# Kernel tuning notes

Hardware: AMD Instinct MI355X
Metric: run time of the kernel (lower is better)

Reference implementation:

```python
import jax, jax.numpy as jnp
import numpy as np

B_SCENES = 2; K = 5; C = 128; H = 64; W = 64
D_INNER = C; D_STATE = 16; DT_RANK = 8
C_TUKEY = 0.3; ALPHA = 2.0; BETA = 0.4; GAMMA = 0.8


def affine_grid(theta, Ho, Wo):
    # torch F.affine_grid, align_corners=False (pixel centers)
    xs = (jnp.arange(Wo, dtype=jnp.float32) + 0.5) * (2.0 / Wo) - 1.0
    ys = (jnp.arange(Ho, dtype=jnp.float32) + 0.5) * (2.0 / Ho) - 1.0
    gx, gy = jnp.meshgrid(xs, ys)
    base = jnp.stack([gx, gy, jnp.ones_like(gx)], axis=-1)  # (H,W,3)
    return jnp.einsum('nij,hwj->nhwi', theta, base)  # (N,H,W,2)


def grid_sample(src, grid):
    # bilinear, zero padding, align_corners=False; src (N,C,H,W), grid (N,H,W,2)
    N, Cc, Hs, Ws = src.shape
    ix = ((grid[..., 0] + 1.0) * Ws - 1.0) * 0.5
    iy = ((grid[..., 1] + 1.0) * Hs - 1.0) * 0.5
    x0 = jnp.floor(ix); y0 = jnp.floor(iy)
    def tap(xf, yf):
        v = ((xf >= 0) & (xf <= Ws - 1) & (yf >= 0) & (yf <= Hs - 1)).astype(src.dtype)
        xc = jnp.clip(xf, 0, Ws - 1).astype(jnp.int32)
        yc = jnp.clip(yf, 0, Hs - 1).astype(jnp.int32)
        vals = jax.vmap(lambda s, y, x: s[:, y, x])(src, yc, xc)  # (N,C,H,W)
        return vals * v[:, None]
    wx1 = (ix - x0)[:, None]; wy1 = (iy - y0)[:, None]
    wx0 = 1.0 - wx1; wy0 = 1.0 - wy1
    return (tap(x0, y0) * wx0 * wy0 + tap(x0 + 1.0, y0) * wx1 * wy0
            + tap(x0, y0 + 1.0) * wx0 * wy1 + tap(x0 + 1.0, y0 + 1.0) * wx1 * wy1)


def ss2d(tokens, in_proj_w, conv_w, conv_b, x_proj_w, dt_w, dt_b, A_logs, Ds, ln_g, ln_b, out_proj_w):
    # tokens (C, Hs, Ws) channel-first; VMamba-style v05_noz core, d_inner=C
    xin = jnp.einsum('chw,dc->dhw', tokens, in_proj_w)
    xc = jax.lax.conv_general_dilated(xin[None], conv_w, (1, 1), [(1, 1), (1, 1)],
                                      dimension_numbers=('NCHW', 'OIHW', 'NCHW'),
                                      feature_group_count=D_INNER)[0] + conv_b[:, None, None]
    xa = jax.nn.silu(xc)
    d, Hs, Ws = xa.shape
    L = Hs * Ws
    x_hw = xa.reshape(d, L)
    x_wh = jnp.swapaxes(xa, 1, 2).reshape(d, L)
    xs = jnp.stack([x_hw, x_wh, x_hw[:, ::-1], x_wh[:, ::-1]], axis=0)  # (4,d,L)
    x_dbl = jnp.einsum('kdl,kcd->kcl', xs, x_proj_w)
    dt = x_dbl[:, :DT_RANK]
    Bm = x_dbl[:, DT_RANK:DT_RANK + D_STATE]
    Cm = x_dbl[:, DT_RANK + D_STATE:]
    dts = jax.nn.softplus(jnp.einsum('kdr,krl->kdl', dt_w, dt) + dt_b[..., None])
    A = -jnp.exp(A_logs)  # (4,d,n)
    seq = (jnp.moveaxis(xs, -1, 0), jnp.moveaxis(dts, -1, 0),
           jnp.moveaxis(Bm, -1, 0), jnp.moveaxis(Cm, -1, 0))
    def step(h, inp):
        xt, dtt, Bt, Ct = inp
        h = h * jnp.exp(dtt[..., None] * A) + (dtt * xt)[..., None] * Bt[:, None, :]
        return h, jnp.einsum('kdn,kn->kd', h, Ct)
    h0 = jnp.zeros((4, d, D_STATE), tokens.dtype)
    _, ys = jax.lax.scan(jax.checkpoint(step), h0, seq)  # ys (L,4,d)
    ys = jnp.moveaxis(ys, 0, -1) + Ds[..., None] * xs  # (4,d,L)
    untr = lambda y: jnp.swapaxes(y.reshape(d, Ws, Hs), 1, 2).reshape(d, L)
    y = ys[0] + untr(ys[1]) + ys[2][:, ::-1] + untr(ys[3][:, ::-1])
    yt = y.T  # (L,d)
    mu = yt.mean(-1, keepdims=True)
    var = ((yt - mu) ** 2).mean(-1, keepdims=True)
    yn = (yt - mu) * jax.lax.rsqrt(var + 1e-5) * ln_g + ln_b
    out = yn @ out_proj_w.T  # (L,C)
    return jnp.moveaxis(out.reshape(Hs, Ws, -1), -1, 0)  # (C,Hs,Ws)


def forward(x, nam, in_proj_w, conv_w, conv_b, x_proj_w, dt_w, dt_b, A_logs, Ds, ln_g, ln_b, out_proj_w):
    xg = x.reshape(B_SCENES, K, C, H, W)  # record_len is constant K
    t_rows = nam[:, 0]  # ego row i=0 of t_matrix: (B,K,2,3)
    def scene(xb, t_row):
        warped = grid_sample(xb, affine_grid(t_row, H, W))  # (K,C,H,W)
        ego = warped[0]
        # per-pixel cosine sim across channels (F.normalize(dim=0) on (C,HW) views)
        en = ego / jnp.maximum(jnp.sqrt((ego ** 2).sum(0, keepdims=True)), 1e-6)
        nb = warped / jnp.maximum(jnp.sqrt((warped ** 2).sum(1, keepdims=True)), 1e-6)
        sims = jnp.clip((en[None] * nb).sum(1), -1.0, 1.0)  # (K,H,W)
        r = jnp.maximum(1.0 - sims, 0.0)
        xr = jnp.maximum(r / C_TUKEY, 0.0)
        w_pix = jnp.maximum(jnp.maximum(1.0 - xr * xr, 0.0) ** 2, 1e-6)[:, None]  # (K,1,H,W)
        tx = t_row[:, 0, 2]; ty = t_row[:, 1, 2]
        yaw = jnp.abs(jnp.arctan2(t_row[:, 0, 1], t_row[:, 0, 0]))
        g = jax.nn.sigmoid(ALPHA - BETA * jnp.sqrt(tx ** 2 + ty ** 2) - GAMMA * yaw)  # (K,)
        logit = jnp.log(w_pix + 1e-8) + jnp.log(g + 1e-8)[:, None, None, None]
        alpha = jax.nn.softmax(logit, axis=0)  # softmax over K per pixel
        weighted = warped * alpha
        tokens = jnp.swapaxes(weighted.reshape(K, C, H * W), 0, 1)  # (C,K,HW)
        out = ss2d(tokens, in_proj_w, conv_w, conv_b, x_proj_w, dt_w, dt_b,
                   A_logs, Ds, ln_g, ln_b, out_proj_w)  # (C,K,HW)
        return jnp.swapaxes(out, 0, 1).reshape(K, C, W, H)[0]  # (C,W,H) as in original view
    return jax.vmap(scene)(xg, t_rows)


def setup_inputs() -> dict:
    key = jax.random.key(0)
    ks = jax.random.split(key, 10)
    x = jax.random.normal(ks[0], (B_SCENES * K, C, H, W), jnp.float32)
    record_len = jnp.full((B_SCENES,), K, dtype=jnp.int32)
    eye = jnp.broadcast_to(jnp.array([[1.0, 0.0, 0.0], [0.0, 1.0, 0.0]], jnp.float32),
                           (B_SCENES, K, K, 2, 3))
    nam = eye + 0.05 * jax.random.normal(ks[1], (B_SCENES, K, K, 2, 3), jnp.float32)
    in_proj_w = 0.05 * jax.random.normal(ks[2], (D_INNER, C), jnp.float32)
    conv_w = 0.1 * jax.random.normal(ks[3], (D_INNER, 1, 3, 3), jnp.float32)
    conv_b = jnp.zeros((D_INNER,), jnp.float32)
    x_proj_w = 0.05 * jax.random.normal(ks[4], (4, DT_RANK + 2 * D_STATE, D_INNER), jnp.float32)
    dt_w = 0.1 * jax.random.normal(ks[5], (4, D_INNER, DT_RANK), jnp.float32)
    dt_b = -4.6 + 0.5 * jax.random.normal(ks[6], (4, D_INNER), jnp.float32)
    A_logs = jnp.broadcast_to(jnp.log(jnp.arange(1, D_STATE + 1, dtype=jnp.float32)),
                              (4, D_INNER, D_STATE)) + jnp.zeros((4, D_INNER, D_STATE), jnp.float32)
    Ds = jnp.ones((4, D_INNER), jnp.float32)
    ln_g = jnp.ones((D_INNER,), jnp.float32)
    ln_b = jnp.zeros((D_INNER,), jnp.float32)
    out_proj_w = 0.05 * jax.random.normal(ks[7], (C, D_INNER), jnp.float32)
    return {"x": x, "record_len": record_len, "normalized_affine_matrix": nam,
            "in_proj_w": in_proj_w, "conv_w": conv_w, "conv_b": conv_b,
            "x_proj_w": x_proj_w, "dt_w": dt_w, "dt_b": dt_b, "A_logs": A_logs,
            "Ds": Ds, "ln_g": ln_g, "ln_b": ln_b, "out_proj_w": out_proj_w}


def reference(x, record_len, normalized_affine_matrix, in_proj_w, conv_w, conv_b,
              x_proj_w, dt_w, dt_b, A_logs, Ds, ln_g, ln_b, out_proj_w):
    # record_len is a constant (= K per scene) and only determines the static grouping
    return forward(x, normalized_affine_matrix, in_proj_w, conv_w, conv_b,
                   x_proj_w, dt_w, dt_b, A_logs, Ds, ln_g, ln_b, out_proj_w)
```

## Files before the change

kernel.cpp:

```cpp
#include <hip/hip_runtime.h>
#include <math.h>

#define B_S   2
#define PIX   4096
#define LL    20480
#define NS    16
#define RR    8
#define NCHK  512
#define LC    40
#define SUBS  10
#define NSUB  4
#define NGRP  32
#define GCH   16
#define K0CH  104

typedef float v2f __attribute__((ext_vector_type(2)));

__device__ __forceinline__ v2f pk_mul(v2f a, v2f b) {
  v2f d;
  asm("v_pk_mul_f32 %0, %1, %2" : "=v"(d) : "v"(a), "v"(b));
  return d;
}
#define PK_FMA_ACC(a, b, c) asm("v_pk_fma_f32 %0, %1, %2, %0" : "+v"(a) : "v"(b), "v"(c))
#define PK_DECAY(h, e, m) asm("v_pk_fma_f32 %0, %0, %1, %2" : "+v"(h) : "v"(e), "v"(m))

template<int K>
__device__ __forceinline__ int zmapT(int l) {
  if (K == 0) return l;
  if (K == 1) return ((l % 5) << 12) + l / 5;
  if (K == 2) return 20479 - l;
  int lr = 20479 - l;
  return ((lr % 5) << 12) + lr / 5;
}

__global__ __launch_bounds__(256)
void k_warp(const float* __restrict__ x, const float* __restrict__ nam,
            float* __restrict__ warped) {
  int g = blockIdx.x * 256 + threadIdx.x;
  int p  = g & 4095;
  int c  = (g >> 12) & 127;
  int bk = g >> 19;
  int b = bk / 5, k = bk - b * 5;
  const float* th = nam + (size_t)(b * 25 + k) * 6;
  float gx = ((p & 63) + 0.5f) * 0.03125f - 1.0f;
  float gy = ((p >> 6) + 0.5f) * 0.03125f - 1.0f;
  float grx = th[0] * gx + th[1] * gy + th[2];
  float gry = th[3] * gx + th[4] * gy + th[5];
  float ix = ((grx + 1.0f) * 64.0f - 1.0f) * 0.5f;
  float iy = ((gry + 1.0f) * 64.0f - 1.0f) * 0.5f;
  float x0 = floorf(ix), y0 = floorf(iy);
  float fx = ix - x0,  fy = iy - y0;
  const float* src = x + (size_t)(bk * 128 + c) * PIX;
  float acc = 0.0f;
  #pragma unroll
  for (int dy = 0; dy < 2; ++dy) {
    float yf = y0 + dy;
    float wy = dy ? fy : 1.0f - fy;
    if (yf < 0.0f || yf > 63.0f) continue;
    int yi = (int)yf;
    #pragma unroll
    for (int dx = 0; dx < 2; ++dx) {
      float xf = x0 + dx;
      float wx = dx ? fx : 1.0f - fx;
      if (xf < 0.0f || xf > 63.0f) continue;
      acc += wx * wy * src[yi * 64 + (int)xf];
    }
  }
  warped[g] = acc;
}

__global__ __launch_bounds__(512)
void k_alpha(const float* __restrict__ warped, const float* __restrict__ nam,
             float* __restrict__ alpha) {
  __shared__ float part[8][64][9];
  int blk = blockIdx.x;
  int b = blk >> 6;
  int p0 = (blk & 63) << 6;
  int wv = threadIdx.x >> 6, lane = threadIdx.x & 63;
  int p = p0 + lane;
  const float* wb = warped + (size_t)b * 5 * 128 * PIX + p;
  float dot[5] = {0,0,0,0,0}, ssq[5] = {0,0,0,0,0};
  int c0 = wv * 16;
  for (int c = c0; c < c0 + 16; ++c) {
    float w0 = wb[(size_t)c * PIX];
    ssq[0] += w0 * w0;
    #pragma unroll
    for (int k = 1; k < 5; ++k) {
      float wk = wb[((size_t)k * 128 + c) * PIX];
      dot[k] += w0 * wk;
      ssq[k] += wk * wk;
    }
  }
  part[wv][lane][0] = ssq[0];
  #pragma unroll
  for (int k = 1; k < 5; ++k) {
    part[wv][lane][k] = dot[k];
    part[wv][lane][4 + k] = ssq[k];
  }
  __syncthreads();
  if (threadIdx.x < 64) {
    float q[9];
    #pragma unroll
    for (int j = 0; j < 9; ++j) {
      float s = 0.0f;
      #pragma unroll
      for (int w = 0; w < 8; ++w) s += part[w][lane][j];
      q[j] = s;
    }
    float n0 = fmaxf(sqrtf(q[0]), 1e-6f);
    float logit[5];
    #pragma unroll
    for (int k = 0; k < 5; ++k) {
      float dotk = (k == 0) ? q[0] : q[k];
      float ssqk = (k == 0) ? q[0] : q[4 + k];
      float nk = fmaxf(sqrtf(ssqk), 1e-6f);
      float sim = fminf(fmaxf(dotk / (n0 * nk), -1.0f), 1.0f);
      float r = fmaxf(1.0f - sim, 0.0f);
      float xr = r * (1.0f / 0.3f);
      float tt = fmaxf(1.0f - xr * xr, 0.0f);
      float wp = fmaxf(tt * tt, 1e-6f);
      const float* th = nam + (size_t)(b * 25 + k) * 6;
      float tx = th[2], ty = th[5];
      float yaw = fabsf(atan2f(th[1], th[0]));
      float gk = 1.0f / (1.0f + __expf(-(2.0f - 0.4f * sqrtf(tx*tx + ty*ty) - 0.8f * yaw)));
      logit[k] = __logf(wp + 1e-8f) + __logf(gk + 1e-8f);
    }
    float m = logit[0];
    #pragma unroll
    for (int k = 1; k < 5; ++k) m = fmaxf(m, logit[k]);
    float e[5], s = 0.0f;
    #pragma unroll
    for (int k = 0; k < 5; ++k) { e[k] = __expf(logit[k] - m); s += e[k]; }
    float inv = 1.0f / s;
    #pragma unroll
    for (int k = 0; k < 5; ++k)
      alpha[((size_t)(b * 5 + k)) * PIX + p] = e[k] * inv;
  }
}

__global__ __launch_bounds__(256, 4)
void k_gemm_in(const float* __restrict__ warped, const float* __restrict__ alpha,
               const float* __restrict__ W, float* __restrict__ X0) {
  __shared__ float xl[64][129];
  __shared__ __align__(16) float wlT[32][132];
  int t = threadIdx.x;
  int row0 = blockIdx.x * 64;
  int b = row0 / LL;
  int z0 = row0 - b * LL;
  int a = z0 >> 12;
  int p0 = z0 & 4095;
  int ba = b * 5 + a;
// ... 92 lines not shown
}

__global__ __launch_bounds__(256, 4)
void k_gemmZ(const float* __restrict__ X, const float* __restrict__ W,
             float* __restrict__ ZdtB, float* __restrict__ ZC) {
  __shared__ float xl[64][129];
  __shared__ __align__(16) float wlT[32][164];
  int t = threadIdx.x;
  int row0 = blockIdx.x * 64;
  #pragma unroll
  for (int i = 0; i < 32; ++i) {
    int idx = i * 256 + t;
    xl[idx >> 7][idx & 127] = X[((size_t)row0 + (idx >> 7)) * 128 + (idx & 127)];
  }
  int zl2 = t & 31;
  int mg  = t >> 5;
  float acc0[20], acc1[20];
  #pragma unroll
  for (int i = 0; i < 20; ++i) { acc0[i] = 0.0f; acc1[i] = 0.0f; }
  for (int c0 = 0; c0 < 128; c0 += 32) {
    __syncthreads();
    #pragma unroll
    for (int i = 0; i < 20; ++i) {
      int m = (t >> 5) * 20 + i;
      wlT[t & 31][m] = W[(size_t)m * 128 + c0 + (t & 31)];
    }
    __syncthreads();
    const float* xr0 = xl[2 * zl2];
    const float* xr1 = xl[2 * zl2 + 1];
    for (int cc = 0; cc < 32; ++cc) {
      float xv0 = xr0[c0 + cc];
      float xv1 = xr1[c0 + cc];
      const float4* wr = (const float4*)(&wlT[cc][mg * 20]);
      #pragma unroll
      for (int q = 0; q < 5; ++q) {
        float4 w4 = wr[q];
        acc0[q*4+0] = fmaf(w4.x, xv0, acc0[q*4+0]);
        acc0[q*4+1] = fmaf(w4.y, xv0, acc0[q*4+1]);
        acc0[q*4+2] = fmaf(w4.z, xv0, acc0[q*4+2]);
        acc0[q*4+3] = fmaf(w4.w, xv0, acc0[q*4+3]);
        acc1[q*4+0] = fmaf(w4.x, xv1, acc1[q*4+0]);
        acc1[q*4+1] = fmaf(w4.y, xv1, acc1[q*4+1]);
        acc1[q*4+2] = fmaf(w4.z, xv1, acc1[q*4+2]);
        acc1[q*4+3] = fmaf(w4.w, xv1, acc1[q*4+3]);
      }
    }
  }
  int dir = mg >> 1;
  int halfc = mg & 1;
  #pragma unroll
  for (int rr = 0; rr < 2; ++rr) {
    const float* acc = rr ? acc1 : acc0;
    int row = row0 + 2 * zl2 + rr;
    int b = row / LL, z = row - b * LL;
    int a = z >> 12, qq = z & 4095;
    int l;
    if (dir == 0)      l = z;
    else if (dir == 1) l = 5 * qq + a;
    else if (dir == 2) l = 20479 - z;
    else               l = 20479 - (5 * qq + a);
    size_t seqrow = (size_t)(b * 4 + dir) * LL + l;
    if (halfc == 0) {
      float* dD = ZdtB + seqrow * 24;
      #pragma unroll
      for (int q2 = 0; q2 < 5; ++q2)
        *(float4*)(dD + q2 * 4) = make_float4(acc[q2*4], acc[q2*4+1], acc[q2*4+2], acc[q2*4+3]);
    } else {
      float* dD = ZdtB + seqrow * 24;
      *(float4*)(dD + 20) = make_float4(acc[0], acc[1], acc[2], acc[3]);
      float* dC = ZC + seqrow * 16;
      #pragma unroll
      for (int q2 = 0; q2 < 4; ++q2)
        *(float4*)(dC + q2 * 4) = make_float4(acc[4+q2*4], acc[4+q2*4+1], acc[4+q2*4+2], acc[4+q2*4+3]);
    }
  }
}

template<int K>
__device__ void scan_body(int b, int chunk, int dh, int lane,
    const float* __restrict__ XT, const float* __restrict__ ZdtB,
    const float* __restrict__ ZC,
    const float* __restrict__ dt_w, const float* __restrict__ dt_b,
    const float* __restrict__ A_logs, const float* __restrict__ Ds,
    float* __restrict__ h_out, float* __restrict__ sumdts,
    float* __restrict__ ysz, float* __restrict__ cumqv,
    float* stD, float* stC)
{
  const int d = dh * 64 + lane;
  const int kd = K * 128 + d;
  bool chainok = true;
  #pragma unroll
  for (int n = 0; n < NS; ++n) {
    float An = -__expf(A_logs[(size_t)kd * 16 + n]);
    chainok = chainok && (fabsf(An + (float)(n + 1)) < 3e-5f * (float)(n + 1));
  }
  v2f dw2[4];
  #pragma unroll
  for (int r = 0; r < 4; ++r) {
    dw2[r][0] = dt_w[(size_t)kd * 8 + 2 * r];
    dw2[r][1] = dt_w[(size_t)kd * 8 + 2 * r + 1];
  }
  const float dtb = dt_b[kd], dsv = Ds[kd];
  v2f h2[8];
  #pragma unroll
  for (int n = 0; n < 8; ++n) h2[n] = (v2f){0.0f, 0.0f};
  float sdt = 0.0f;
  float qrun = 1.0f;
  const int seq = b * 4 + K;
  const float* ZDs = ZdtB + (size_t)seq * LL * 24;
  const float* ZCs = ZC + (size_t)seq * LL * 16;
  const float* Xb = XT + (size_t)b * LL * 128;
  float* ysb = ysz + (size_t)seq * PIX * 128;
  float* cqb = cumqv + (size_t)seq * PIX * 128;
  const int l0 = chunk * LC;

  if (__all(chainok ? 1 : 0)) {
    #pragma unroll 1
    for (int sub = 0; sub < NSUB; ++sub) {
      const int ls = l0 + sub * SUBS;
      {
        const v2f* srcD = (const v2f*)(ZDs + (size_t)ls * 24);
        v2f* dstD = (v2f*)stD;
        #pragma unroll
        for (int i = 0; i < 2; ++i) {
          int idx = i * 64 + lane;
          if (idx < SUBS * 12) dstD[idx] = srcD[idx];
        }
      }
      int s0c = 0;
      bool needC;
      if (K == 0)      needC = (ls < PIX);
      else if (K == 2) needC = (ls + SUBS > LL - PIX);
      else             needC = true;
      if (K == 1) s0c = (5 - (ls % 5)) % 5;
      if (K == 3) s0c = (9 - (ls % 5)) % 5;
      if (needC) {
        if (K == 0 || K == 2) {
          const v2f* srcC = (const v2f*)(ZCs + (size_t)ls * 16);
          v2f* dstC = (v2f*)stC;
          #pragma unroll
          for (int i = 0; i < 2; ++i) {
            int idx = i * 64 + lane;
            if (idx < SUBS * 8) dstC[idx] = srcC[idx];
          }
        } else {
          int j = lane >> 4, col = lane & 15;
          if (j < 2) {
            int l = ls + s0c + 5 * j;
            if (l > LL - 1) l = LL - 1;
            stC[lane] = ZCs[(size_t)l * 16 + col];
          }
        }
      }
      float xr[SUBS];
      #pragma unroll
      for (int s = 0; s < SUBS; ++s) {
        int z = zmapT<K>(ls + s);
        xr[s] = Xb[(size_t)z * 128 + d];
      }
      int zc = 0;
      if (K == 1) zc = (ls + s0c) / 5;
      if (K == 3) zc = (20479 - ls - s0c) / 5;
      int yj = 0;
      #pragma unroll
      for (int s = 0; s < SUBS; ++s) {
        const v2f* rowD = (const v2f*)(stD + s * 24);
        v2f zd0 = rowD[0], zd1 = rowD[1], zd2 = rowD[2], zd3 = rowD[3];
        v2f da = pk_mul(dw2[0], zd0);
        PK_FMA_ACC(da, dw2[1], zd1);
        PK_FMA_ACC(da, dw2[2], zd2);
        PK_FMA_ACC(da, dw2[3], zd3);
        float dtl = dtb + da[0] + da[1];
        float edt = __expf(dtl);
        float e1 = __builtin_amdgcn_rcpf(1.0f + edt);
        float dt = (dtl > 20.0f) ? dtl : __logf(1.0f + edt);
        sdt += dt;
        qrun *= e1;
        float xsv = xr[s];
        float dtx = dt * xsv;
        v2f dtx2 = {dtx, dtx};
        float e2 = e1 * e1;
        v2f E[8];
        E[0] = (v2f){e1, e2};
        v2f e2s = {e2, e2};
        E[1] = pk_mul(E[0], e2s);
        E[2] = pk_mul(E[1], e2s);
        E[3] = pk_mul(E[2], e2s);
        float e8 = E[3][1];
        v2f e8s = {e8, e8};
        E[4] = pk_mul(E[0], e8s);
        E[5] = pk_mul(E[1], e8s);
        E[6] = pk_mul(E[2], e8s);
        E[7] = pk_mul(E[3], e8s);
        const v2f* B2 = (const v2f*)(stD + s * 24 + 8);
        #pragma unroll
        for (int i = 0; i < 8; ++i) {
          v2f m = pk_mul(dtx2, B2[i]);
          PK_DECAY(h2[i], E[i], m);
        }
        bool doY;
        int z;
        if (K == 0)      { z = ls + s;            doY = (z < PIX); }
        else if (K == 2) { z = 20479 - (ls + s);  doY = (z < PIX); }
        else             { z = zc;                doY = ((s % 5) == s0c); }
        if (doY) {
          const v2f* C2 = (const v2f*)(stC + ((K == 0 || K == 2) ? s : yj) * 16);
          v2f ya = pk_mul(h2[0], C2[0]);
          #pragma unroll
          for (int i = 1; i < 8; ++i) PK_FMA_ACC(ya, h2[i], C2[i]);
          float y = fmaf(dsv, xsv, ya[0] + ya[1]);
          size_t o = (size_t)z * 128 + d;
          ysb[o] = y;
          cqb[o] = qrun;
          ++yj;
          if (K == 1) ++zc;
          if (K == 3) --zc;
        }
      }
    }
  } else {
    float An[NS];
    #pragma unroll
    for (int n = 0; n < NS; ++n) An[n] = -__expf(A_logs[(size_t)kd * 16 + n]);
    float hs[NS];
    #pragma unroll
    for (int n = 0; n < NS; ++n) hs[n] = 0.0f;
    #pragma unroll 1
    for (int l = l0; l < l0 + LC; ++l) {
      int z = zmapT<K>(l);
      const float* rowD = ZDs + (size_t)l * 24;
      float dtl = dtb;
      #pragma unroll
      for (int r = 0; r < RR; ++r) dtl += dt_w[(size_t)kd * 8 + r] * rowD[r];
      float edt = __expf(dtl);
      float dt = (dtl > 20.0f) ? dtl : __logf(1.0f + edt);
      sdt += dt;
      float xv = Xb[(size_t)z * 128 + d];
      float dtx = dt * xv;
      #pragma unroll
      for (int n = 0; n < NS; ++n)
        hs[n] = hs[n] * __expf(dt * An[n]) + dtx * rowD[8 + n];
      if (z < PIX) {
        const float* rowC = ZCs + (size_t)l * 16;
        float y = dsv * xv;
        #pragma unroll
        for (int n = 0; n < NS; ++n) y = fmaf(hs[n], rowC[n], y);
        size_t o = (size_t)z * 128 + d;
        ysb[o] = y;
        cqb[o] = __expf(-sdt);
      }
    }
    #pragma unroll
    for (int n = 0; n < 8; ++n) h2[n] = (v2f){hs[2*n], hs[2*n+1]};
  }
  float* ho = h_out + (((size_t)seq * NCHK + chunk) * 128 + d) * 16;
  #pragma unroll
  for (int n = 0; n < 8; ++n) {
    ho[2*n] = h2[n][0];
    ho[2*n+1] = h2[n][1];
  }
  sumdts[((size_t)seq * NCHK + chunk) * 128 + d] = sdt;
}

__global__ __launch_bounds__(128, 8)
void k_scan1(const float* __restrict__ XT, const float* __restrict__ ZdtB,
             const float* __restrict__ ZC,
             const float* __restrict__ dt_w, const float* __restrict__ dt_b,
             const float* __restrict__ A_logs, const float* __restrict__ Ds,
             float* __restrict__ h_out, float* __restrict__ sumdts,
             float* __restrict__ ysz, float* __restrict__ cumqv) {
  __shared__ __align__(16) float stD_all[2][SUBS * 24];
  __shared__ __align__(16) float stC_all[2][SUBS * 16];
  int tid = threadIdx.x, wid = tid >> 6, lane = tid & 63;
  int bid = blockIdx.x;
  int bb = bid / (K0CH + 3 * NCHK);
  int idx = bid - bb * (K0CH + 3 * NCHK);
  int k, chunk;
  if (idx < K0CH)                 { k = 0; chunk = idx; }
  else if (idx < K0CH + NCHK)     { k = 1; chunk = idx - K0CH; }
  else if (idx < K0CH + 2 * NCHK) { k = 2; chunk = idx - (K0CH + NCHK); }
  else                            { k = 3; chunk = idx - (K0CH + 2 * NCHK); }
  int dh = wid;
  float* stD = stD_all[wid];
  float* stC = stC_all[wid];
  switch (k) {
    case 0: scan_body<0>(bb, chunk, dh, lane, XT, ZdtB, ZC, dt_w, dt_b, A_logs, Ds, h_out, sumdts, ysz, cumqv, stD, stC); break;
    case 1: scan_body<1>(bb, chunk, dh, lane, XT, ZdtB, ZC, dt_w, dt_b, A_logs, Ds, h_out, sumdts, ysz, cumqv, stD, stC); break;
    case 2: scan_body<2>(bb, chunk, dh, lane, XT, ZdtB, ZC, dt_w, dt_b, A_logs, Ds, h_out, sumdts, ysz, cumqv, stD, stC); break;
    default: scan_body<3>(bb, chunk, dh, lane, XT, ZdtB, ZC, dt_w, dt_b, A_logs, Ds, h_out, sumdts, ysz, cumqv, stD, stC); break;
  }
}

__global__ __launch_bounds__(256)
void k_comb_a(const float* __restrict__ A_logs, const float* __restrict__ sumdts,
              const float* __restrict__ h_out, float* __restrict__ Ag,
              float* __restrict__ Bg) {
  int g = blockIdx.x * 256 + threadIdx.x;
  int n = g & 15;
  int d = (g >> 4) & 127;
  int grp = (g >> 11) & 31;
  int seq = g >> 16;
  int k = seq & 3;
  if (k == 0 && grp > 6) return;
  float An = -__expf(A_logs[(size_t)(k * 128 + d) * 16 + n]);
  float A = 1.0f, Bv = 0.0f;
  size_t cbase = (size_t)seq * NCHK + grp * GCH;
  #pragma unroll 4
  for (int j = 0; j < GCH; ++j) {
    float a = __expf(An * sumdts[(cbase + j) * 128 + d]);
    float b = h_out[((cbase + j) * 128 + d) * 16 + n];
    A *= a;
    Bv = Bv * a + b;
  }
  size_t o = (((size_t)seq * NGRP + grp) * 128 + d) * 16 + n;
  Ag[o] = A;
  Bg[o] = Bv;
}

__global__ __launch_bounds__(256)
void k_comb_b(const float* __restrict__ Ag, const float* __restrict__ Bg,
              float* __restrict__ Hg) {
  int g = blockIdx.x * 256 + threadIdx.x;
  int n = g & 15;
  int d = (g >> 4) & 127;
  int seq = g >> 11;
  float H = 0.0f;
  #pragma unroll
  for (int grp = 0; grp < NGRP; ++grp) {
    size_t o = (((size_t)seq * NGRP + grp) * 128 + d) * 16 + n;
    Hg[o] = H;
    H = Ag[o] * H + Bg[o];
  }
}

__global__ __launch_bounds__(256)
void k_comb_c(const float* __restrict__ A_logs, const float* __restrict__ sumdts,
              const float* __restrict__ h_out, const float* __restrict__ Hg,
              float* __restrict__ h_in) {
  int g = blockIdx.x * 256 + threadIdx.x;
  int n = g & 15;
  int d = (g >> 4) & 127;
  int grp = (g >> 11) & 31;
  int seq = g >> 16;
  int k = seq & 3;
  if (k == 0 && grp > 6) return;
  if (k == 2 && grp < 25) return;
  float An = -__expf(A_logs[(size_t)(k * 128 + d) * 16 + n]);
  float h = Hg[(((size_t)seq * NGRP + grp) * 128 + d) * 16 + n];
  size_t cbase = (size_t)seq * NCHK + grp * GCH;
  #pragma unroll 4
  for (int j = 0; j < GCH; ++j) {
    size_t o = ((cbase + j) * 128 + d) * 16 + n;
    h_in[o] = h;
    float a = __expf(An * sumdts[(cbase + j) * 128 + d]);
    h = a * h + h_out[o];
  }
}

__global__ __launch_bounds__(256)
void k_wt(const float* __restrict__ Wo, float* __restrict__ WT) {
  __shared__ float tl[32][33];
  int bx = blockIdx.x & 3, by = blockIdx.x >> 2;
  int t = threadIdx.x;
  int tx = t & 31, ty = t >> 5;
  #pragma unroll
  for (int i = 0; i < 4; ++i)
    tl[ty + i * 8][tx] = Wo[(size_t)(by * 32 + ty + i * 8) * 128 + bx * 32 + tx];
  __syncthreads();
  #pragma unroll
  for (int i = 0; i < 4; ++i)
    WT[(size_t)(bx * 32 + ty + i * 8) * 128 + by * 32 + tx] = tl[tx][ty + i * 8];
}

__global__ __launch_bounds__(256)
void k_merge(const float* __restrict__ ysz, const float* __restrict__ ZC,
             const float* __restrict__ A_logs, const float* __restrict__ h_in,
             const float* __restrict__ cumq,
             const float* __restrict__ ln_g, const float* __restrict__ ln_b,
             const float* __restrict__ WT, float* __restrict__ out) {
  __shared__ __align__(16) float ynT[128][20];
  __shared__ float red[4][8][2];
  int blk = blockIdx.x;
  int b = blk >> 8;
  int p0 = (blk & 255) * 16;
  int tid = threadIdx.x;
  int t = tid & 127;
  int half = tid >> 7;
  int w = tid >> 6;
  float g = ln_g[t], bb = ln_b[t];
  bool cok[4];
  #pragma unroll
  for (int k = 0; k < 4; ++k) {
    bool c = true;
    #pragma unroll
    for (int n = 0; n < NS; ++n) {
      float An = -__expf(A_logs[(size_t)(k * 128 + t) * 16 + n]);
      c = c && (fabsf(An + (float)(n + 1)) < 3e-5f * (float)(n + 1));
    }
    cok[k] = c;
  }
  float yv[8];
  #pragma unroll
  for (int i = 0; i < 8; ++i) {
    int p = p0 + 2 * i + half;
    float y = 0.0f;
    #pragma unroll
    for (int k = 0; k < 4; ++k) {
      size_t zi = ((size_t)(b * 4 + k) * PIX + p) * 128 + t;
      float yk = ysz[zi];
      int l;
      if (k == 0)      l = p;
      else if (k == 1) l = 5 * p;
      else if (k == 2) l = 20479 - p;
      else             l = 20479 - 5 * p;
      int chunk = l / LC;
      float q = cumq[zi];
      const v2f* hi2 = (const v2f*)(h_in + (((size_t)(b * 4 + k) * NCHK + chunk) * 128 + t) * 16);
      const v2f* Cr2 = (const v2f*)(ZC + ((size_t)(b * 4 + k) * LL + l) * 16);
      float fix;
      if (cok[k]) {
        float q2 = q * q;
        v2f Q[8];
        Q[0] = (v2f){q, q2};
        v2f q2s = {q2, q2};
        Q[1] = pk_mul(Q[0], q2s);
        Q[2] = pk_mul(Q[1], q2s);
        Q[3] = pk_mul(Q[2], q2s);
        float q8 = Q[3][1];
        v2f q8s = {q8, q8};
        Q[4] = pk_mul(Q[0], q8s);
        Q[5] = pk_mul(Q[1], q8s);
        Q[6] = pk_mul(Q[2], q8s);
        Q[7] = pk_mul(Q[3], q8s);
        v2f a = pk_mul(pk_mul(hi2[0], Cr2[0]), Q[0]);
        #pragma unroll
        for (int j = 1; j < 8; ++j) {
          v2f m = pk_mul(hi2[j], Cr2[j]);
          PK_FMA_ACC(a, m, Q[j]);
        }
        fix = a[0] + a[1];
      } else {
        float cd = -__logf(q);
        fix = 0.0f;
        const float* hi = (const float*)hi2;
        const float* Cr = (const float*)Cr2;
        #pragma unroll
        for (int n = 0; n < NS; ++n) {
          float An = -__expf(A_logs[(size_t)(k * 128 + t) * 16 + n]);
          fix += Cr[n] * hi[n] * __expf(An * cd);
        }
      }
      y += yk + fix;
    }
    yv[i] = y;
    float s1 = y, s2 = y * y;
    #pragma unroll
    for (int off = 32; off; off >>= 1) {
      s1 += __shfl_xor(s1, off);
      s2 += __shfl_xor(s2, off);
    }
    if ((tid & 63) == 0) { red[w][i][0] = s1; red[w][i][1] = s2; }
  }
  __syncthreads();
  #pragma unroll
  for (int i = 0; i < 8; ++i) {
    int pl = 2 * i + half;
    float S1 = red[half * 2][i][0] + red[half * 2 + 1][i][0];
    float S2 = red[half * 2][i][1] + red[half * 2 + 1][i][1];
    float mu = S1 * (1.0f / 128.0f);
    float var = S2 * (1.0f / 128.0f) - mu * mu;
    float rs = rsqrtf(var + 1e-5f);
    ynT[t][pl] = (yv[i] - mu) * rs * g + bb;
  }
  __syncthreads();
  float acc[8];
  #pragma unroll
  for (int i = 0; i < 8; ++i) acc[i] = 0.0f;
  for (int dd = 0; dd < 128; ++dd) {
    float wv = WT[(size_t)dd * 128 + t];
    const float4* yr = (const float4*)(&ynT[dd][half * 8]);
    float4 ya = yr[0], yb4 = yr[1];
    acc[0] = fmaf(ya.x,  wv, acc[0]);
    acc[1] = fmaf(ya.y,  wv, acc[1]);
    acc[2] = fmaf(ya.z,  wv, acc[2]);
    acc[3] = fmaf(ya.w,  wv, acc[3]);
    acc[4] = fmaf(yb4.x, wv, acc[4]);
    acc[5] = fmaf(yb4.y, wv, acc[5]);
    acc[6] = fmaf(yb4.z, wv, acc[6]);
    acc[7] = fmaf(yb4.w, wv, acc[7]);
  }
  float* dst = out + ((size_t)b * 128 + t) * PIX + p0 + half * 8;
  *(float4*)(dst)     = make_float4(acc[0], acc[1], acc[2], acc[3]);
  *(float4*)(dst + 4) = make_float4(acc[4], acc[5], acc[6], acc[7]);
}

extern "C" void kernel_launch(void* const* d_in, const int* in_sizes, int n_in,
                              void* d_out, int out_size, void* d_ws, size_t ws_size,
                              hipStream_t stream) {
  const float* x         = (const float*)d_in[0];
  const float* nam       = (const float*)d_in[2];
  const float* in_proj_w = (const float*)d_in[3];
  const float* conv_w    = (const float*)d_in[4];
  const float* conv_b    = (const float*)d_in[5];
  const float* x_proj_w  = (const float*)d_in[6];
  const float* dt_w      = (const float*)d_in[7];
  const float* dt_b      = (const float*)d_in[8];
  const float* A_logs    = (const float*)d_in[9];
  const float* Ds        = (const float*)d_in[10];
  const float* ln_g      = (const float*)d_in[11];
  const float* ln_b      = (const float*)d_in[12];
  const float* out_proj_w= (const float*)d_in[13];
  float* out = (float*)d_out;
  float* ws  = (float*)d_ws;

  float* warped = ws;
  float* alpha  = warped + 5242880;
  float* X0     = alpha  + 40960;
  float* XT     = X0     + 5242880;
  float* ZdtB   = XT     + 5242880;
  float* ZC     = ZdtB   + 3932160;
  float* sums   = ZC     + 2621440;
  float* ysz    = sums   + 524288;
  float* cumq   = ysz    + 4194304;
  float* WT     = cumq   + 4194304;
  float* Ag     = WT     + 16384;
  float* Bg     = Ag     + 524288;
  float* Hg     = Bg     + 524288;

  float* h_out = ws;
  float* h_in  = XT;

  k_warp   <<<20480, 256, 0, stream>>>(x, nam, warped);
  k_alpha  <<<128,   512, 0, stream>>>(warped, nam, alpha);
  k_gemm_in<<<640,   256, 0, stream>>>(warped, alpha, in_proj_w, X0);
  k_conv   <<<5120,  256, 0, stream>>>(X0, conv_w, conv_b, XT);
  k_gemmZ  <<<640,   256, 0, stream>>>(XT, x_proj_w, ZdtB, ZC);
  k_scan1  <<<B_S * (K0CH + 3 * NCHK), 128, 0, stream>>>(XT, ZdtB, ZC, dt_w, dt_b,
                                                         A_logs, Ds, h_out, sums, ysz, cumq);
  k_comb_a <<<2048,  256, 0, stream>>>(A_logs, sums, h_out, Ag, Bg);
  k_comb_b <<<64,    256, 0, stream>>>(Ag, Bg, Hg);
  k_comb_c <<<2048,  256, 0, stream>>>(A_logs, sums, h_out, Hg, h_in);
  k_wt     <<<16,    256, 0, stream>>>(out_proj_w, WT);
  k_merge  <<<512,   256, 0, stream>>>(ysz, ZC, A_logs, h_in, cumq,
                                       ln_g, ln_b, WT, out);
}
```

Before: 254.8 us.

## Shrink scan chunk length, share warp sampling weights, compact h_in layout

The scan chunk length drops from 40 to 32, which raises the chunk and group counts and grows the workspace. The combine and merge kernels now use a compact h_in layout that keeps only the chunks actually read. k_warp computes bilinear weights and indices once per pixel tile in shared memory and reuses them across 4 channels, replacing the per-thread coordinate math and branches. More chunks give more parallelism per sequence but add carry-combine work and memory traffic.

```diff
diff --git a/kernel.cpp b/kernel.cpp
--- a/kernel.cpp
+++ b/kernel.cpp
@@ -6,13 +6,13 @@
 #define LL    20480
 #define NS    16
 #define RR    8
-#define NCHK  512
-#define LC    40
-#define SUBS  10
+#define NCHK  640
+#define LC    32
+#define SUBS  8
 #define NSUB  4
-#define NGRP  32
+#define NGRP  40
 #define GCH   16
-#define K0CH  104
+#define K0CH  128
 
 typedef float v2f __attribute__((ext_vector_type(2)));
 
@@ -36,37 +36,52 @@
 __global__ __launch_bounds__(256)
 void k_warp(const float* __restrict__ x, const float* __restrict__ nam,
             float* __restrict__ warped) {
-  int g = blockIdx.x * 256 + threadIdx.x;
-  int p  = g & 4095;
-  int c  = (g >> 12) & 127;
-  int bk = g >> 19;
-  int b = bk / 5, k = bk - b * 5;
-  const float* th = nam + (size_t)(b * 25 + k) * 6;
-  float gx = ((p & 63) + 0.5f) * 0.03125f - 1.0f;
-  float gy = ((p >> 6) + 0.5f) * 0.03125f - 1.0f;
-  float grx = th[0] * gx + th[1] * gy + th[2];
-  float gry = th[3] * gx + th[4] * gy + th[5];
-  float ix = ((grx + 1.0f) * 64.0f - 1.0f) * 0.5f;
-  float iy = ((gry + 1.0f) * 64.0f - 1.0f) * 0.5f;
-  float x0 = floorf(ix), y0 = floorf(iy);
-  float fx = ix - x0,  fy = iy - y0;
+  __shared__ float wL[4][64];
+  __shared__ int   iL[4][64];
+  int blk = blockIdx.x;
+  int bk = blk >> 11;
+  int rem = blk & 2047;
+  int ct = rem >> 6, pt = rem & 63;
+  int p0 = pt * 64;
+  int t = threadIdx.x;
+  int pl = t & 63, cg = t >> 6;
+  if (t < 64) {
+    int b = bk / 5, k = bk - b * 5;
+    const float* th = nam + (size_t)(b * 25 + k) * 6;
+    int p = p0 + t;
+    float gx = ((p & 63) + 0.5f) * 0.03125f - 1.0f;
+    float gy = ((p >> 6) + 0.5f) * 0.03125f - 1.0f;
+    float grx = th[0] * gx + th[1] * gy + th[2];
+    float gry = th[3] * gx + th[4] * gy + th[5];
+    float ix = ((grx + 1.0f) * 64.0f - 1.0f) * 0.5f;
+    float iy = ((gry + 1.0f) * 64.0f - 1.0f) * 0.5f;
+    float x0 = floorf(ix), y0 = floorf(iy);
+    float fx = ix - x0, fy = iy - y0;
+    float vx0 = (x0 >= 0.0f && x0 <= 63.0f) ? 1.0f : 0.0f;
+    float vx1 = (x0 >= -1.0f && x0 <= 62.0f) ? 1.0f : 0.0f;
+    float vy0 = (y0 >= 0.0f && y0 <= 63.0f) ? 1.0f : 0.0f;
+    float vy1 = (y0 >= -1.0f && y0 <= 62.0f) ? 1.0f : 0.0f;
+    int xi0 = (int)fminf(fmaxf(x0, 0.0f), 63.0f);
+    int yi0 = (int)fminf(fmaxf(y0, 0.0f), 63.0f);
+    int xi1 = (int)fminf(fmaxf(x0 + 1.0f, 0.0f), 63.0f);
+    int yi1 = (int)fminf(fmaxf(y0 + 1.0f, 0.0f), 63.0f);
+    wL[0][t] = (1.0f - fx) * (1.0f - fy) * vx0 * vy0;
+    wL[1][t] = fx * (1.0f - fy) * vx1 * vy0;
+    wL[2][t] = (1.0f - fx) * fy * vx0 * vy1;
+    wL[3][t] = fx * fy * vx1 * vy1;
+    iL[0][t] = yi0 * 64 + xi0;
+    iL[1][t] = yi0 * 64 + xi1;
+    iL[2][t] = yi1 * 64 + xi0;
+    iL[3][t] = yi1 * 64 + xi1;
+  }
+  __syncthreads();
+  int c = ct * 4 + cg;
   const float* src = x + (size_t)(bk * 128 + c) * PIX;
-  float acc = 0.0f;
-  #pragma unroll
-  for (int dy = 0; dy < 2; ++dy) {
-    float yf = y0 + dy;
-    float wy = dy ? fy : 1.0f - fy;
-    if (yf < 0.0f || yf > 63.0f) continue;
-    int yi = (int)yf;
-    #pragma unroll
-    for (int dx = 0; dx < 2; ++dx) {
-      float xf = x0 + dx;
-      float wx = dx ? fx : 1.0f - fx;
-      if (xf < 0.0f || xf > 63.0f) continue;
-      acc += wx * wy * src[yi * 64 + (int)xf];
-    }
-  }
-  warped[g] = acc;
+  float acc = wL[0][pl] * src[iL[0][pl]]
+            + wL[1][pl] * src[iL[1][pl]]
+            + wL[2][pl] * src[iL[2][pl]]
+            + wL[3][pl] * src[iL[3][pl]];
+  warped[((size_t)(bk * 128 + c)) * PIX + p0 + pl] = acc;
 }
 
 __global__ __launch_bounds__(512)
@@ -516,13 +531,13 @@
   __shared__ __align__(16) float stC_all[2][SUBS * 16];
   int tid = threadIdx.x, wid = tid >> 6, lane = tid & 63;
   int bid = blockIdx.x;
-  int bb = bid / (K0CH + 3 * NCHK);
-  int idx = bid - bb * (K0CH + 3 * NCHK);
+  int bb = bid >> 11;
+  int idx = bid & 2047;
   int k, chunk;
-  if (idx < K0CH)                 { k = 0; chunk = idx; }
-  else if (idx < K0CH + NCHK)     { k = 1; chunk = idx - K0CH; }
-  else if (idx < K0CH + 2 * NCHK) { k = 2; chunk = idx - (K0CH + NCHK); }
-  else                            { k = 3; chunk = idx - (K0CH + 2 * NCHK); }
+  if (idx < K0CH)        { k = 0; chunk = idx; }
+  else if (idx < 768)    { k = 1; chunk = idx - K0CH; }
+  else if (idx < 1408)   { k = 2; chunk = idx - 768; }
+  else                   { k = 3; chunk = idx - 1408; }
   int dh = wid;
   float* stD = stD_all[wid];
   float* stC = stC_all[wid];
@@ -541,10 +556,11 @@
   int g = blockIdx.x * 256 + threadIdx.x;
   int n = g & 15;
   int d = (g >> 4) & 127;
-  int grp = (g >> 11) & 31;
-  int seq = g >> 16;
+  int rem = g >> 11;
+  int seq = rem / NGRP;
+  int grp = rem - seq * NGRP;
   int k = seq & 3;
-  if (k == 0 && grp > 6) return;
+  if (k == 0 && grp > 7) return;
   float An = -__expf(A_logs[(size_t)(k * 128 + d) * 16 + n]);
   float A = 1.0f, Bv = 0.0f;
   size_t cbase = (size_t)seq * NCHK + grp * GCH;
@@ -583,21 +599,27 @@
   int g = blockIdx.x * 256 + threadIdx.x;
   int n = g & 15;
   int d = (g >> 4) & 127;
-  int grp = (g >> 11) & 31;
-  int seq = g >> 16;
+  int rem = g >> 11;
+  int seq = rem / NGRP;
+  int grp = rem - seq * NGRP;
   int k = seq & 3;
-  if (k == 0 && grp > 6) return;
-  if (k == 2 && grp < 25) return;
+  if (k == 0 && grp > 7) return;
+  if (k == 2 && grp < 32) return;
+  int b = seq >> 2;
+  int cstart = (k == 2) ? 512 : 0;
+  int offk = (k == 0) ? 0 : (k == 1) ? 128 : (k == 2) ? 768 : 896;
   float An = -__expf(A_logs[(size_t)(k * 128 + d) * 16 + n]);
   float h = Hg[(((size_t)seq * NGRP + grp) * 128 + d) * 16 + n];
   size_t cbase = (size_t)seq * NCHK + grp * GCH;
   #pragma unroll 4
   for (int j = 0; j < GCH; ++j) {
-    size_t o = ((cbase + j) * 128 + d) * 16 + n;
-    h_in[o] = h;
-    float a = __expf(An * sumdts[(cbase + j) * 128 + d]);
-    h = a * h + h_out[o];
-  }
+    int chunk = grp * GCH + j;
+    size_t o = ((size_t)seq * NCHK + chunk) * 128 + d;
+    h_in[(((size_t)b * 1536 + offk + (chunk - cstart)) * 128 + d) * 16 + n] = h;
+    float a = __expf(An * sumdts[o]);
+    h = a * h + h_out[o * 16 + n];
+  }
+  (void)cbase;
 }
 
 __global__ __launch_bounds__(256)
@@ -657,8 +679,10 @@
       else if (k == 2) l = 20479 - p;
       else             l = 20479 - 5 * p;
       int chunk = l / LC;
+      int cidx = chunk - ((k == 2) ? 512 : 0);
+      int offk = (k == 0) ? 0 : (k == 1) ? 128 : (k == 2) ? 768 : 896;
       float q = cumq[zi];
-      const v2f* hi2 = (const v2f*)(h_in + (((size_t)(b * 4 + k) * NCHK + chunk) * 128 + t) * 16);
+      const v2f* hi2 = (const v2f*)(h_in + (((size_t)b * 1536 + offk + cidx) * 128 + t) * 16);
       const v2f* Cr2 = (const v2f*)(ZC + ((size_t)(b * 4 + k) * LL + l) * 16);
       float fix;
       if (cok[k]) {
@@ -763,12 +787,12 @@
   float* ZdtB   = XT     + 5242880;
   float* ZC     = ZdtB   + 3932160;
   float* sums   = ZC     + 2621440;
-  float* ysz    = sums   + 524288;
+  float* ysz    = sums   + 655360;
   float* cumq   = ysz    + 4194304;
   float* WT     = cumq   + 4194304;
   float* Ag     = WT     + 16384;
-  float* Bg     = Ag     + 524288;
-  float* Hg     = Bg     + 524288;
+  float* Bg     = Ag     + 655360;
+  float* Hg     = Bg     + 655360;
 
   float* h_out = ws;
   float* h_in  = XT;
@@ -778,11 +802,11 @@
   k_gemm_in<<<640,   256, 0, stream>>>(warped, alpha, in_proj_w, X0);
   k_conv   <<<5120,  256, 0, stream>>>(X0, conv_w, conv_b, XT);
   k_gemmZ  <<<640,   256, 0, stream>>>(XT, x_proj_w, ZdtB, ZC);
-  k_scan1  <<<B_S * (K0CH + 3 * NCHK), 128, 0, stream>>>(XT, ZdtB, ZC, dt_w, dt_b,
-                                                         A_logs, Ds, h_out, sums, ysz, cumq);
-  k_comb_a <<<2048,  256, 0, stream>>>(A_logs, sums, h_out, Ag, Bg);
+  k_scan1  <<<B_S * 2048, 128, 0, stream>>>(XT, ZdtB, ZC, dt_w, dt_b,
+                                            A_logs, Ds, h_out, sums, ysz, cumq);
+  k_comb_a <<<2560,  256, 0, stream>>>(A_logs, sums, h_out, Ag, Bg);
   k_comb_b <<<64,    256, 0, stream>>>(Ag, Bg, Hg);
-  k_comb_c <<<2048,  256, 0, stream>>>(A_logs, sums, h_out, Hg, h_in);
+  k_comb_c <<<2560,  256, 0, stream>>>(A_logs, sums, h_out, Hg, h_in);
   k_wt     <<<16,    256, 0, stream>>>(out_proj_w, WT);
   k_merge  <<<512,   256, 0, stream>>>(ysz, ZC, A_logs, h_in, cumq,
                                        ln_g, ln_b, WT, out);
```

Measured after the change: 256.9 us. Within noise of the previous version (+0.9%).

## Share warp coordinates per pixel tile, precompute chain flags, widen scan loads

Applied to the files above, without the earlier changes.

k_warp now computes the bilinear indices and weights once per 64-pixel tile in shared memory and reuses them across 4 channels per block, instead of recomputing them per channel thread. The per-lane A_logs chain check (16 exps per thread) in k_scan1 and k_merge is replaced by flags computed once in extra blocks of k_wt, which now runs first. Scan staging copies and shared reads use float4 vectors, and dt_w is kept in registers for the tail loop. The new flag kernel ordering adds a dependency, and the block-level sync in k_warp adds a small serialization.

```diff
diff --git a/kernel.cpp b/kernel.cpp
--- a/kernel.cpp
+++ b/kernel.cpp
@@ -15,6 +15,7 @@
 #define K0CH  104
 
 typedef float v2f __attribute__((ext_vector_type(2)));
+typedef float v4f __attribute__((ext_vector_type(4)));
 
 __device__ __forceinline__ v2f pk_mul(v2f a, v2f b) {
   v2f d;
@@ -36,37 +37,52 @@
 __global__ __launch_bounds__(256)
 void k_warp(const float* __restrict__ x, const float* __restrict__ nam,
             float* __restrict__ warped) {
-  int g = blockIdx.x * 256 + threadIdx.x;
-  int p  = g & 4095;
-  int c  = (g >> 12) & 127;
-  int bk = g >> 19;
-  int b = bk / 5, k = bk - b * 5;
-  const float* th = nam + (size_t)(b * 25 + k) * 6;
-  float gx = ((p & 63) + 0.5f) * 0.03125f - 1.0f;
-  float gy = ((p >> 6) + 0.5f) * 0.03125f - 1.0f;
-  float grx = th[0] * gx + th[1] * gy + th[2];
-  float gry = th[3] * gx + th[4] * gy + th[5];
-  float ix = ((grx + 1.0f) * 64.0f - 1.0f) * 0.5f;
-  float iy = ((gry + 1.0f) * 64.0f - 1.0f) * 0.5f;
-  float x0 = floorf(ix), y0 = floorf(iy);
-  float fx = ix - x0,  fy = iy - y0;
+  __shared__ float wL[4][64];
+  __shared__ int   iL[4][64];
+  int blk = blockIdx.x;
+  int bk = blk >> 11;
+  int rem = blk & 2047;
+  int ct = rem >> 6, pt = rem & 63;
+  int p0 = pt * 64;
+  int t = threadIdx.x;
+  int pl = t & 63, cg = t >> 6;
+  if (t < 64) {
+    int b = bk / 5, k = bk - b * 5;
+    const float* th = nam + (size_t)(b * 25 + k) * 6;
+    int p = p0 + t;
+    float gx = ((p & 63) + 0.5f) * 0.03125f - 1.0f;
+    float gy = ((p >> 6) + 0.5f) * 0.03125f - 1.0f;
+    float grx = th[0] * gx + th[1] * gy + th[2];
+    float gry = th[3] * gx + th[4] * gy + th[5];
+    float ix = ((grx + 1.0f) * 64.0f - 1.0f) * 0.5f;
+    float iy = ((gry + 1.0f) * 64.0f - 1.0f) * 0.5f;
+    float x0 = floorf(ix), y0 = floorf(iy);
+    float fx = ix - x0, fy = iy - y0;
+    float vx0 = (x0 >= 0.0f && x0 <= 63.0f) ? 1.0f : 0.0f;
+    float vx1 = (x0 >= -1.0f && x0 <= 62.0f) ? 1.0f : 0.0f;
+    float vy0 = (y0 >= 0.0f && y0 <= 63.0f) ? 1.0f : 0.0f;
+    float vy1 = (y0 >= -1.0f && y0 <= 62.0f) ? 1.0f : 0.0f;
+    int xi0 = (int)fminf(fmaxf(x0, 0.0f), 63.0f);
+    int yi0 = (int)fminf(fmaxf(y0, 0.0f), 63.0f);
+    int xi1 = (int)fminf(fmaxf(x0 + 1.0f, 0.0f), 63.0f);
+    int yi1 = (int)fminf(fmaxf(y0 + 1.0f, 0.0f), 63.0f);
+    wL[0][t] = (1.0f - fx) * (1.0f - fy) * vx0 * vy0;
+    wL[1][t] = fx * (1.0f - fy) * vx1 * vy0;
+    wL[2][t] = (1.0f - fx) * fy * vx0 * vy1;
+    wL[3][t] = fx * fy * vx1 * vy1;
+    iL[0][t] = yi0 * 64 + xi0;
+    iL[1][t] = yi0 * 64 + xi1;
+    iL[2][t] = yi1 * 64 + xi0;
+    iL[3][t] = yi1 * 64 + xi1;
+  }
+  __syncthreads();
+  int c = ct * 4 + cg;
   const float* src = x + (size_t)(bk * 128 + c) * PIX;
-  float acc = 0.0f;
-  #pragma unroll
-  for (int dy = 0; dy < 2; ++dy) {
-    float yf = y0 + dy;
-    float wy = dy ? fy : 1.0f - fy;
-    if (yf < 0.0f || yf > 63.0f) continue;
-    int yi = (int)yf;
-    #pragma unroll
-    for (int dx = 0; dx < 2; ++dx) {
-      float xf = x0 + dx;
-      float wx = dx ? fx : 1.0f - fx;
-      if (xf < 0.0f || xf > 63.0f) continue;
-      acc += wx * wy * src[yi * 64 + (int)xf];
-    }
-  }
-  warped[g] = acc;
+  float acc = wL[0][pl] * src[iL[0][pl]]
+            + wL[1][pl] * src[iL[1][pl]]
+            + wL[2][pl] * src[iL[2][pl]]
+            + wL[3][pl] * src[iL[3][pl]];
+  warped[((size_t)(bk * 128 + c)) * PIX + p0 + pl] = acc;
 }
 
 __global__ __launch_bounds__(512)
@@ -325,24 +341,17 @@
     const float* __restrict__ ZC,
     const float* __restrict__ dt_w, const float* __restrict__ dt_b,
     const float* __restrict__ A_logs, const float* __restrict__ Ds,
+    const int* __restrict__ chainflags,
     float* __restrict__ h_out, float* __restrict__ sumdts,
     float* __restrict__ ysz, float* __restrict__ cumqv,
     float* stD, float* stC)
 {
   const int d = dh * 64 + lane;
   const int kd = K * 128 + d;
-  bool chainok = true;
-  #pragma unroll
-  for (int n = 0; n < NS; ++n) {
-    float An = -__expf(A_logs[(size_t)kd * 16 + n]);
-    chainok = chainok && (fabsf(An + (float)(n + 1)) < 3e-5f * (float)(n + 1));
-  }
-  v2f dw2[4];
-  #pragma unroll
-  for (int r = 0; r < 4; ++r) {
-    dw2[r][0] = dt_w[(size_t)kd * 8 + 2 * r];
-    dw2[r][1] = dt_w[(size_t)kd * 8 + 2 * r + 1];
-  }
+  bool chainok = chainflags[kd] != 0;
+  float dw[8];
+  #pragma unroll
+  for (int r = 0; r < 8; ++r) dw[r] = dt_w[(size_t)kd * 8 + r];
   const float dtb = dt_b[kd], dsv = Ds[kd];
   v2f h2[8];
   #pragma unroll
@@ -362,13 +371,8 @@
     for (int sub = 0; sub < NSUB; ++sub) {
       const int ls = l0 + sub * SUBS;
       {
-        const v2f* srcD = (const v2f*)(ZDs + (size_t)ls * 24);
-        v2f* dstD = (v2f*)stD;
-        #pragma unroll
-        for (int i = 0; i < 2; ++i) {
-          int idx = i * 64 + lane;
-          if (idx < SUBS * 12) dstD[idx] = srcD[idx];
-        }
+        const v4f* srcD = (const v4f*)(ZDs + (size_t)ls * 24);
+        if (lane < SUBS * 6) ((v4f*)stD)[lane] = srcD[lane];
       }
       int s0c = 0;
       bool needC;
@@ -379,19 +383,13 @@
       if (K == 3) s0c = (9 - (ls % 5)) % 5;
       if (needC) {
         if (K == 0 || K == 2) {
-          const v2f* srcC = (const v2f*)(ZCs + (size_t)ls * 16);
-          v2f* dstC = (v2f*)stC;
-          #pragma unroll
-          for (int i = 0; i < 2; ++i) {
-            int idx = i * 64 + lane;
-            if (idx < SUBS * 8) dstC[idx] = srcC[idx];
-          }
+          const v4f* srcC = (const v4f*)(ZCs + (size_t)ls * 16);
+          if (lane < SUBS * 4) ((v4f*)stC)[lane] = srcC[lane];
         } else {
-          int j = lane >> 4, col = lane & 15;
-          if (j < 2) {
-            int l = ls + s0c + 5 * j;
+          if (lane < 8) {
+            int l = ls + s0c + 5 * (lane >> 2);
             if (l > LL - 1) l = LL - 1;
-            stC[lane] = ZCs[(size_t)l * 16 + col];
+            ((v4f*)stC)[lane] = *(const v4f*)(ZCs + (size_t)l * 16 + (lane & 3) * 4);
           }
         }
       }
@@ -407,13 +405,13 @@
       int yj = 0;
       #pragma unroll
       for (int s = 0; s < SUBS; ++s) {
-        const v2f* rowD = (const v2f*)(stD + s * 24);
-        v2f zd0 = rowD[0], zd1 = rowD[1], zd2 = rowD[2], zd3 = rowD[3];
-        v2f da = pk_mul(dw2[0], zd0);
-        PK_FMA_ACC(da, dw2[1], zd1);
-        PK_FMA_ACC(da, dw2[2], zd2);
-        PK_FMA_ACC(da, dw2[3], zd3);
-        float dtl = dtb + da[0] + da[1];
+        const v4f* rowD4 = (const v4f*)(stD + s * 24);
+        v4f rA = rowD4[0], rB = rowD4[1];
+        float dtl = dtb;
+        dtl = fmaf(dw[0], rA[0], dtl); dtl = fmaf(dw[1], rA[1], dtl);
+        dtl = fmaf(dw[2], rA[2], dtl); dtl = fmaf(dw[3], rA[3], dtl);
+        dtl = fmaf(dw[4], rB[0], dtl); dtl = fmaf(dw[5], rB[1], dtl);
+        dtl = fmaf(dw[6], rB[2], dtl); dtl = fmaf(dw[7], rB[3], dtl);
         float edt = __expf(dtl);
         float e1 = __builtin_amdgcn_rcpf(1.0f + edt);
         float dt = (dtl > 20.0f) ? dtl : __logf(1.0f + edt);
@@ -435,22 +433,32 @@
         E[5] = pk_mul(E[1], e8s);
         E[6] = pk_mul(E[2], e8s);
         E[7] = pk_mul(E[3], e8s);
-        const v2f* B2 = (const v2f*)(stD + s * 24 + 8);
-        #pragma unroll
-        for (int i = 0; i < 8; ++i) {
-          v2f m = pk_mul(dtx2, B2[i]);
-          PK_DECAY(h2[i], E[i], m);
-        }
+        v4f B0 = rowD4[2], B1 = rowD4[3], B2v = rowD4[4], B3 = rowD4[5];
+        v2f m;
+        m = pk_mul(dtx2, (v2f){B0[0], B0[1]});  PK_DECAY(h2[0], E[0], m);
+        m = pk_mul(dtx2, (v2f){B0[2], B0[3]});  PK_DECAY(h2[1], E[1], m);
+        m = pk_mul(dtx2, (v2f){B1[0], B1[1]});  PK_DECAY(h2[2], E[2], m);
+        m = pk_mul(dtx2, (v2f){B1[2], B1[3]});  PK_DECAY(h2[3], E[3], m);
+        m = pk_mul(dtx2, (v2f){B2v[0], B2v[1]}); PK_DECAY(h2[4], E[4], m);
+        m = pk_mul(dtx2, (v2f){B2v[2], B2v[3]}); PK_DECAY(h2[5], E[5], m);
+        m = pk_mul(dtx2, (v2f){B3[0], B3[1]});  PK_DECAY(h2[6], E[6], m);
+        m = pk_mul(dtx2, (v2f){B3[2], B3[3]});  PK_DECAY(h2[7], E[7], m);
         bool doY;
         int z;
         if (K == 0)      { z = ls + s;            doY = (z < PIX); }
         else if (K == 2) { z = 20479 - (ls + s);  doY = (z < PIX); }
         else             { z = zc;                doY = ((s % 5) == s0c); }
         if (doY) {
-          const v2f* C2 = (const v2f*)(stC + ((K == 0 || K == 2) ? s : yj) * 16);
-          v2f ya = pk_mul(h2[0], C2[0]);
-          #pragma unroll
-          for (int i = 1; i < 8; ++i) PK_FMA_ACC(ya, h2[i], C2[i]);
+          const v4f* C4 = (const v4f*)(stC + ((K == 0 || K == 2) ? s : yj) * 16);
+          v4f C0 = C4[0], C1 = C4[1], C2v = C4[2], C3 = C4[3];
+          v2f ya = pk_mul(h2[0], (v2f){C0[0], C0[1]});
+          PK_FMA_ACC(ya, h2[1], ((v2f){C0[2], C0[3]}));
+          PK_FMA_ACC(ya, h2[2], ((v2f){C1[0], C1[1]}));
+          PK_FMA_ACC(ya, h2[3], ((v2f){C1[2], C1[3]}));
+          PK_FMA_ACC(ya, h2[4], ((v2f){C2v[0], C2v[1]}));
+          PK_FMA_ACC(ya, h2[5], ((v2f){C2v[2], C2v[3]}));
+          PK_FMA_ACC(ya, h2[6], ((v2f){C3[0], C3[1]}));
+          PK_FMA_ACC(ya, h2[7], ((v2f){C3[2], C3[3]}));
           float y = fmaf(dsv, xsv, ya[0] + ya[1]);
           size_t o = (size_t)z * 128 + d;
           ysb[o] = y;
@@ -474,7 +482,7 @@
       const float* rowD = ZDs + (size_t)l * 24;
       float dtl = dtb;
       #pragma unroll
-      for (int r = 0; r < RR; ++r) dtl += dt_w[(size_t)kd * 8 + r] * rowD[r];
+      for (int r = 0; r < RR; ++r) dtl += dw[r] * rowD[r];
       float edt = __expf(dtl);
       float dt = (dtl > 20.0f) ? dtl : __logf(1.0f + edt);
       sdt += dt;
@@ -510,6 +518,7 @@
              const float* __restrict__ ZC,
              const float* __restrict__ dt_w, const float* __restrict__ dt_b,
              const float* __restrict__ A_logs, const float* __restrict__ Ds,
+             const int* __restrict__ chainflags,
              float* __restrict__ h_out, float* __restrict__ sumdts,
              float* __restrict__ ysz, float* __restrict__ cumqv) {
   __shared__ __align__(16) float stD_all[2][SUBS * 24];
@@ -527,10 +536,10 @@
   float* stD = stD_all[wid];
   float* stC = stC_all[wid];
   switch (k) {
-    case 0: scan_body<0>(bb, chunk, dh, lane, XT, ZdtB, ZC, dt_w, dt_b, A_logs, Ds, h_out, sumdts, ysz, cumqv, stD, stC); break;
-    case 1: scan_body<1>(bb, chunk, dh, lane, XT, ZdtB, ZC, dt_w, dt_b, A_logs, Ds, h_out, sumdts, ysz, cumqv, stD, stC); break;
-    case 2: scan_body<2>(bb, chunk, dh, lane, XT, ZdtB, ZC, dt_w, dt_b, A_logs, Ds, h_out, sumdts, ysz, cumqv, stD, stC); break;
-    default: scan_body<3>(bb, chunk, dh, lane, XT, ZdtB, ZC, dt_w, dt_b, A_logs, Ds, h_out, sumdts, ysz, cumqv, stD, stC); break;
+    case 0: scan_body<0>(bb, chunk, dh, lane, XT, ZdtB, ZC, dt_w, dt_b, A_logs, Ds, chainflags, h_out, sumdts, ysz, cumqv, stD, stC); break;
+    case 1: scan_body<1>(bb, chunk, dh, lane, XT, ZdtB, ZC, dt_w, dt_b, A_logs, Ds, chainflags, h_out, sumdts, ysz, cumqv, stD, stC); break;
+    case 2: scan_body<2>(bb, chunk, dh, lane, XT, ZdtB, ZC, dt_w, dt_b, A_logs, Ds, chainflags, h_out, sumdts, ysz, cumqv, stD, stC); break;
+    default: scan_body<3>(bb, chunk, dh, lane, XT, ZdtB, ZC, dt_w, dt_b, A_logs, Ds, chainflags, h_out, sumdts, ysz, cumqv, stD, stC); break;
   }
 }
 
@@ -601,7 +610,19 @@
 }
 
 __global__ __launch_bounds__(256)
-void k_wt(const float* __restrict__ Wo, float* __restrict__ WT) {
+void k_wt(const float* __restrict__ Wo, float* __restrict__ WT,
+          const float* __restrict__ A_logs, int* __restrict__ chainflags) {
+  if (blockIdx.x >= 16) {
+    int kd = (blockIdx.x - 16) * 256 + threadIdx.x;
+    bool c = true;
+    #pragma unroll
+    for (int n = 0; n < NS; ++n) {
+      float An = -__expf(A_logs[(size_t)kd * 16 + n]);
+      c = c && (fabsf(An + (float)(n + 1)) < 3e-5f * (float)(n + 1));
+    }
+    chainflags[kd] = c ? 1 : 0;
+    return;
+  }
   __shared__ float tl[32][33];
   int bx = blockIdx.x & 3, by = blockIdx.x >> 2;
   int t = threadIdx.x;
@@ -618,7 +639,7 @@
 __global__ __launch_bounds__(256)
 void k_merge(const float* __restrict__ ysz, const float* __restrict__ ZC,
              const float* __restrict__ A_logs, const float* __restrict__ h_in,
-             const float* __restrict__ cumq,
+             const float* __restrict__ cumq, const int* __restrict__ chainflags,
              const float* __restrict__ ln_g, const float* __restrict__ ln_b,
              const float* __restrict__ WT, float* __restrict__ out) {
   __shared__ __align__(16) float ynT[128][20];
@@ -633,15 +654,7 @@
   float g = ln_g[t], bb = ln_b[t];
   bool cok[4];
   #pragma unroll
-  for (int k = 0; k < 4; ++k) {
-    bool c = true;
-    #pragma unroll
-    for (int n = 0; n < NS; ++n) {
-      float An = -__expf(A_logs[(size_t)(k * 128 + t) * 16 + n]);
-      c = c && (fabsf(An + (float)(n + 1)) < 3e-5f * (float)(n + 1));
-    }
-    cok[k] = c;
-  }
+  for (int k = 0; k < 4; ++k) cok[k] = chainflags[k * 128 + t] != 0;
   float yv[8];
   #pragma unroll
   for (int i = 0; i < 8; ++i) {
@@ -769,21 +782,23 @@
   float* Ag     = WT     + 16384;
   float* Bg     = Ag     + 524288;
   float* Hg     = Bg     + 524288;
+  int*   chainflags = (int*)(Hg + 524288);
 
   float* h_out = ws;
   float* h_in  = XT;
 
+  k_wt     <<<18,    256, 0, stream>>>(out_proj_w, WT, A_logs, chainflags);
   k_warp   <<<20480, 256, 0, stream>>>(x, nam, warped);
   k_alpha  <<<128,   512, 0, stream>>>(warped, nam, alpha);
   k_gemm_in<<<640,   256, 0, stream>>>(warped, alpha, in_proj_w, X0);
   k_conv   <<<5120,  256, 0, stream>>>(X0, conv_w, conv_b, XT);
   k_gemmZ  <<<640,   256, 0, stream>>>(XT, x_proj_w, ZdtB, ZC);
   k_scan1  <<<B_S * (K0CH + 3 * NCHK), 128, 0, stream>>>(XT, ZdtB, ZC, dt_w, dt_b,
-                                                         A_logs, Ds, h_out, sums, ysz, cumq);
+                                                         A_logs, Ds, chainflags,
+                                                         h_out, sums, ysz, cumq);
   k_comb_a <<<2048,  256, 0, stream>>>(A_logs, sums, h_out, Ag, Bg);
   k_comb_b <<<64,    256, 0, stream>>>(Ag, Bg, Hg);
   k_comb_c <<<2048,  256, 0, stream>>>(A_logs, sums, h_out, Hg, h_in);
-  k_wt     <<<16,    256, 0, stream>>>(out_proj_w, WT);
-  k_merge  <<<512,   256, 0, stream>>>(ysz, ZC, A_logs, h_in, cumq,
+  k_merge  <<<512,   256, 0, stream>>>(ysz, ZC, A_logs, h_in, cumq, chainflags,
                                        ln_g, ln_b, WT, out);
 }
```

Result: faster. 245.3 us, median of 2 (-3.7%).
